# Kernel optimization log

Measured on AMD Instinct MI355X. Metric: run time of the kernel, lower is better.

## Reference

```python
import jax, jax.numpy as jnp
import numpy as np

H = 2048
V = 32000
B = 4            # 2 chosen + 2 rejected sequences
T = 1024
BETA = 0.1
IGNORE_INDEX = -100


def setup_inputs() -> dict:
    key = jax.random.key(0)
    k1, k2, k3, k4, k5 = jax.random.split(key, 5)
    x = jax.random.normal(k1, (B, T, H), dtype=jnp.float32)
    ref_x = jax.random.normal(k2, (B, T, H), dtype=jnp.float32)
    y = jax.random.randint(k3, (B, T), 0, V, dtype=jnp.int64)
    # Linear weights scaled ~1/sqrt(H) so logits are well-conditioned
    W = jax.random.normal(k4, (V, H), dtype=jnp.float32) * (1.0 / np.sqrt(H))
    W_ref = jax.random.normal(k5, (V, H), dtype=jnp.float32) * (1.0 / np.sqrt(H))
    return {"x": x, "ref_x": ref_x, "y": y, "W": W, "W_ref": W_ref}


def _avg_seq_logps(h, W, y, mask):
    # h: [B,T,H], W: [V,H] -> average per-sequence log-prob of the target tokens
    logits = jnp.einsum("bth,vh->btv", h, W)                 # [B,T,V]
    logps = jax.nn.log_softmax(logits, axis=-1)
    y_safe = jnp.where(mask, y, 0)
    per_tok = jnp.take_along_axis(logps, y_safe[..., None], axis=-1)[..., 0]  # [B,T]
    m = mask.astype(logps.dtype)
    return (per_tok * m).sum(-1) / m.sum(-1)                  # [B]


def reference(x, ref_x, y, W, W_ref):
    mask = y != IGNORE_INDEX
    logps = _avg_seq_logps(x, W, y, mask)
    # reference model path is computed without gradients (torch.no_grad in Liger)
    ref_logps = jax.lax.stop_gradient(_avg_seq_logps(ref_x, W_ref, y, mask))
    half = B // 2
    chosen, rejected = logps[:half], logps[half:]
    ref_chosen, ref_rejected = ref_logps[:half], ref_logps[half:]
    logits_diff = BETA * ((chosen - ref_chosen) - (rejected - ref_rejected))
    loss = -jax.nn.log_sigmoid(logits_diff).sum() / half
    return loss
```

## Files before the change

### kernel.cpp

```cpp
#include <hip/hip_runtime.h>
#include <cstdint>
#include <cstddef>

#define HDIM 2048
#define VOCAB 32000
#define BT 4096
#define NVB 125
#define BETA_F 0.1f
#define SCALE_X 16.0f
#define SCALE_W 64.0f
#define INV_SC (1.0f / (SCALE_X * SCALE_W))

typedef float f32x4 __attribute__((ext_vector_type(4)));
typedef long lx2 __attribute__((ext_vector_type(2)));

__device__ __forceinline__ void async_lds16(const void* g, void* l) {
  __builtin_amdgcn_global_load_lds(
      (__attribute__((address_space(1))) void*)g,
      (__attribute__((address_space(3))) void*)l,
      16, 0, 0);
}

#define BAR() __builtin_amdgcn_s_barrier()
#define SCHED0() __builtin_amdgcn_sched_barrier(0)
#define VMCNT(n) do { asm volatile("s_waitcnt vmcnt(" #n ")" ::: "memory"); \
                      __builtin_amdgcn_sched_barrier(0); } while (0)

__global__ void cast_fp8_kernel(const float* __restrict__ src,
                                uint4* __restrict__ dst, int n16, float scale) {
  int i = blockIdx.x * blockDim.x + threadIdx.x;
  int stride = gridDim.x * blockDim.x;
  for (; i < n16; i += stride) {
    const float4* s = (const float4*)src + (size_t)i * 4;
    uint4 o;
    {
      float4 a = s[0];
      int r = __builtin_amdgcn_cvt_pk_fp8_f32(a.x * scale, a.y * scale, 0, false);
      o.x = __builtin_amdgcn_cvt_pk_fp8_f32(a.z * scale, a.w * scale, r, true);
    }
    {
      float4 a = s[1];
      int r = __builtin_amdgcn_cvt_pk_fp8_f32(a.x * scale, a.y * scale, 0, false);
      o.y = __builtin_amdgcn_cvt_pk_fp8_f32(a.z * scale, a.w * scale, r, true);
    }
    {
      float4 a = s[2];
      int r = __builtin_amdgcn_cvt_pk_fp8_f32(a.x * scale, a.y * scale, 0, false);
      o.z = __builtin_amdgcn_cvt_pk_fp8_f32(a.z * scale, a.w * scale, r, true);
    }
    {
      float4 a = s[3];
      int r = __builtin_amdgcn_cvt_pk_fp8_f32(a.x * scale, a.y * scale, 0, false);
      o.w = __builtin_amdgcn_cvt_pk_fp8_f32(a.z * scale, a.w * scale, r, true);
    }
    dst[i] = o;
  }
}

__global__ __launch_bounds__(1024) void gemm_lse256(
    const unsigned char* __restrict__ Xq,
    const unsigned char* __restrict__ Xrq,
    const unsigned char* __restrict__ Wq,
    const unsigned char* __restrict__ Wrq,
    float2* __restrict__ part) {
  __shared__ __align__(16) char lds[4][2][2][8192];

  const int tid = threadIdx.x;
  const int lane = tid & 63;
  const int w = tid >> 6;
  const int wm = w >> 2;
  const int wn = w & 3;
  const int which = blockIdx.y;

  const int lin = blockIdx.x;
  const int nl = (lin & 7) * 250 + (lin >> 3);
  const int mb = nl & 15;
  const int nb = nl >> 4;

  const unsigned char* A = which ? Xrq : Xq;
  const unsigned char* B = which ? Wrq : Wq;
  float2* pp = part + (size_t)which * BT * NVB;

  const int lanep = lane ^ ((lane & 32) >> 4);
  const int srow = (w >> 3) * 128 + (w & 7) * 16 + (lanep >> 2);
  const int scol = (lanep & 3) * 16;
  const unsigned char* Ag = A + (size_t)(mb * 256 + srow) * HDIM + scol;
  const unsigned char* Bg = B + (size_t)(nb * 256 + srow) * HDIM + scol;

#define STAGE_AB(buf, T) do {                                                 \
    int _t = (T) > 31 ? 31 : (T);                                             \
    async_lds16(Ag + (size_t)_t * 64, &lds[buf][0][0][0] + w * 1024);         \
    async_lds16(Bg + (size_t)_t * 64, &lds[buf][1][0][0] + w * 1024);         \
  } while (0)

  const int l15 = lane & 15;
  const int kbyte = (lane >> 4) * 16;
#define FRAGP(d0, d1, halfptr, row) do {                                      \
    int _r = (row);                                                           \
    int _L = _r * 64 + kbyte;                                                 \
    lx2 _v = *(const lx2*)((halfptr) + (_L ^ (((_r >> 3) & 1) << 5)));        \
    d0 = _v.x; d1 = _v.y;                                                     \
  } while (0)

  const char* Ah[4] = { &lds[0][0][wm >> 1][0], &lds[1][0][wm >> 1][0],
                        &lds[2][0][wm >> 1][0], &lds[3][0][wm >> 1][0] };
  const char* Bh[4] = { &lds[0][1][wn >> 1][0], &lds[1][1][wn >> 1][0],
                        &lds[2][1][wn >> 1][0], &lds[3][1][wn >> 1][0] };
  const int arow = (wm & 1) * 64 + l15;
  const int brow = (wn & 1) * 64 + l15;

  f32x4 acc[4][4] = {};
  long aLo[2][2], aHi[2][2], bLo[2][2], bHi[2][2];

#define RD_ALO(buf) do {                                                      \
    _Pragma("unroll") for (int mi = 0; mi < 2; ++mi)                          \
      FRAGP(aLo[mi][0], aLo[mi][1], Ah[buf], arow + mi * 16);                 \
  } while (0)
#define RD_AHI(buf) do {                                                      \
    _Pragma("unroll") for (int mi = 0; mi < 2; ++mi)                          \
      FRAGP(aHi[mi][0], aHi[mi][1], Ah[buf], arow + (2 + mi) * 16);           \
  } while (0)
#define RD_B01(buf) do {                                                      \
    _Pragma("unroll") for (int ni = 0; ni < 2; ++ni)                          \
      FRAGP(bLo[ni][0], bLo[ni][1], Bh[buf], brow + ni * 16);                 \
  } while (0)
#define RD_B23(buf) do {                                                      \
    _Pragma("unroll") for (int ni = 0; ni < 2; ++ni)                          \
      FRAGP(bHi[ni][0], bHi[ni][1], Bh[buf], brow + (2 + ni) * 16);           \
  } while (0)
#define MFMA_Q(AG, BG, MI0, NI0) do {                                         \
    __builtin_amdgcn_s_setprio(1);                                            \
    _Pragma("unroll") for (int kk = 0; kk < 2; ++kk)                          \
    _Pragma("unroll") for (int mi = 0; mi < 2; ++mi)                          \
    _Pragma("unroll") for (int ni = 0; ni < 2; ++ni)                          \
      acc[(MI0) + mi][(NI0) + ni] = __builtin_amdgcn_mfma_f32_16x16x32_fp8_fp8( \
          AG[mi][kk], BG[ni][kk], acc[(MI0) + mi][(NI0) + ni], 0, 0, 0);      \
    __builtin_amdgcn_s_setprio(0);                                            \
  } while (0)

#define TILE(C, CN, ST) do {                                                  \
    RD_B23(C); SCHED0();                                                      \
    MFMA_Q(aLo, bLo, 0, 0); SCHED0();                                         \
    STAGE_AB((C + 3) & 3, ST);                                                \
    RD_AHI(C); SCHED0();                                                      \
    MFMA_Q(aLo, bHi, 0, 2); SCHED0();                                         \
    MFMA_Q(aHi, bLo, 2, 0); SCHED0();                                         \
    VMCNT(4);                     \
    BAR(); SCHED0();                                                          \
    RD_ALO(CN); RD_B01(CN); SCHED0();                                         \
    MFMA_Q(aHi, bHi, 2, 2); SCHED0();                                         \
  } while (0)

  STAGE_AB(0, 0);
  STAGE_AB(1, 1);
  STAGE_AB(2, 2);
  VMCNT(4);
  BAR(); SCHED0();
  RD_ALO(0); RD_B01(0);
  SCHED0();

  for (int i = 0; i < 8; ++i) {
    const int base = 4 * i;
    TILE(0, 1, base + 3);
    TILE(1, 2, base + 4);
    TILE(2, 3, base + 5);
    TILE(3, 0, base + 6);
  }
  VMCNT(0);
  BAR(); SCHED0();

  float* red = (float*)&lds[0][0][0][0];
#pragma unroll
  for (int mi = 0; mi < 4; ++mi) {
#pragma unroll
    for (int r = 0; r < 4; ++r) {
      float v0 = acc[mi][0][r] * INV_SC;
      float v1 = acc[mi][1][r] * INV_SC;
      float v2 = acc[mi][2][r] * INV_SC;
      float v3 = acc[mi][3][r] * INV_SC;
      float m = fmaxf(fmaxf(v0, v1), fmaxf(v2, v3));
#pragma unroll
      for (int o = 1; o < 16; o <<= 1) m = fmaxf(m, __shfl_xor(m, o, 64));
      float s = __expf(v0 - m) + __expf(v1 - m) + __expf(v2 - m) + __expf(v3 - m);
#pragma unroll
      for (int o = 1; o < 16; o <<= 1) s += __shfl_xor(s, o, 64);
      if (l15 == 0) {
        int row = wm * 64 + mi * 16 + (lane >> 4) * 4 + r;
        red[wn * 256 + row] = m;
        red[1024 + wn * 256 + row] = s;
      }
    }
  }
  __syncthreads();
  if (tid < 256) {
    float m0 = red[tid], m1 = red[256 + tid], m2 = red[512 + tid], m3 = red[768 + tid];
    float M = fmaxf(fmaxf(m0, m1), fmaxf(m2, m3));
    float S = red[1024 + tid] * __expf(m0 - M) + red[1280 + tid] * __expf(m1 - M) +
              red[1536 + tid] * __expf(m2 - M) + red[1792 + tid] * __expf(m3 - M);
    pp[(size_t)(mb * 256 + tid) * NVB + nb] = make_float2(M, S);
  }
#undef STAGE_AB
#undef FRAGP
#undef RD_ALO
#undef RD_AHI
#undef RD_B01
#undef RD_B23
#undef MFMA_Q
#undef TILE
}

__global__ void target_logit(const float* __restrict__ x, const float* __restrict__ xr,
                             const float* __restrict__ W, const float* __restrict__ Wr,
                             const int* __restrict__ y, float* __restrict__ tlog) {
  int wid = (blockIdx.x * blockDim.x + threadIdx.x) >> 6;
  int lane = threadIdx.x & 63;
  int which = wid >> 12;
  int tok = wid & 4095;
  int yy = y[tok];
  int ys = (yy == -100) ? 0 : yy;
  const float* xv = (which ? xr : x) + (size_t)tok * HDIM;
  const float* wv = (which ? Wr : W) + (size_t)ys * HDIM;
  const float4* x4 = (const float4*)xv;
  const float4* w4 = (const float4*)wv;
  float sum = 0.f;
  for (int i = lane; i < HDIM / 4; i += 64) {
    float4 a = x4[i], b = w4[i];
    sum += a.x * b.x + a.y * b.y + a.z * b.z + a.w * b.w;
  }
#pragma unroll
  for (int o = 1; o < 64; o <<= 1) sum += __shfl_xor(sum, o, 64);
  if (lane == 0) tlog[wid] = sum;
}

__global__ void lse_combine(const float2* __restrict__ part,
                            const float* __restrict__ tlog,
                            float* __restrict__ ptok) {
  int wid = (blockIdx.x * blockDim.x + threadIdx.x) >> 6;
  int lane = threadIdx.x & 63;
  const float2* p = part + (size_t)wid * NVB;
  float m = -INFINITY, s = 0.f;
  for (int i = lane; i < NVB; i += 64) {
    float2 v = p[i];
    float M = fmaxf(m, v.x);
    s = s * __expf(m - M) + v.y * __expf(v.x - M);
    m = M;
  }
#pragma unroll
  for (int o = 1; o < 64; o <<= 1) {
    float mo = __shfl_xor(m, o, 64);
    float so = __shfl_xor(s, o, 64);
    float M = fmaxf(m, mo);
    s = s * __expf(m - M) + so * __expf(mo - M);
    m = M;
  }
  if (lane == 0) ptok[wid] = tlog[wid] - (m + logf(s));
}

__global__ void final_loss(const float* __restrict__ ptok,
                           const int* __restrict__ y, float* __restrict__ out) {
  __shared__ float rs[256];
  __shared__ float rc[256];
  __shared__ float seq[8];
  int tid = threadIdx.x;
  for (int s = 0; s < 8; ++s) {
    int which = s >> 2, b = s & 3;
    float lsum = 0.f, lcnt = 0.f;
    for (int t = tid; t < 1024; t += 256) {
      int yy = y[b * 1024 + t];
      if (yy != -100) {
        lsum += ptok[which * 4096 + b * 1024 + t];
        lcnt += 1.f;
      }
    }
    rs[tid] = lsum; rc[tid] = lcnt;
    __syncthreads();
    for (int o = 128; o > 0; o >>= 1) {
      if (tid < o) { rs[tid] += rs[tid + o]; rc[tid] += rc[tid + o]; }
      __syncthreads();
    }
    if (tid == 0) seq[s] = rs[0] / rc[0];
    __syncthreads();
  }
  if (tid == 0) {
    float d0 = BETA_F * ((seq[0] - seq[4]) - (seq[2] - seq[6]));
    float d1 = BETA_F * ((seq[1] - seq[5]) - (seq[3] - seq[7]));
    auto sp = [](float a) { return fmaxf(a, 0.f) + log1pf(expf(-fabsf(a))); };
    out[0] = (sp(-d0) + sp(-d1)) * 0.5f;
  }
}

extern "C" void kernel_launch(void* const* d_in, const int* in_sizes, int n_in,
                              void* d_out, int out_size, void* d_ws, size_t ws_size,
                              hipStream_t stream) {
  const float* x   = (const float*)d_in[0];
  const float* xr  = (const float*)d_in[1];
  const int*   y   = (const int*)d_in[2];
  const float* Wf  = (const float*)d_in[3];
  const float* Wrf = (const float*)d_in[4];
  float* out = (float*)d_out;

  char* ws = (char*)d_ws;
  size_t off = 0;
  auto alloc = [&](size_t bytes) -> void* {
    void* p = ws + off;
    off = (off + bytes + 255) & ~(size_t)255;
    return p;
  };
  unsigned char* Xq  = (unsigned char*)alloc((size_t)BT * HDIM);
  unsigned char* Xrq = (unsigned char*)alloc((size_t)BT * HDIM);
  unsigned char* Wq  = (unsigned char*)alloc((size_t)VOCAB * HDIM);
  unsigned char* Wrq = (unsigned char*)alloc((size_t)VOCAB * HDIM);
  float2* part = (float2*)alloc((size_t)2 * BT * NVB * sizeof(float2));
  float*  tlog = (float*)alloc((size_t)2 * BT * sizeof(float));
  float*  ptok = (float*)alloc((size_t)2 * BT * sizeof(float));

  cast_fp8_kernel<<<2048, 256, 0, stream>>>(x,  (uint4*)Xq,  BT * HDIM / 16, SCALE_X);
  cast_fp8_kernel<<<2048, 256, 0, stream>>>(xr, (uint4*)Xrq, BT * HDIM / 16, SCALE_X);
  cast_fp8_kernel<<<2048, 256, 0, stream>>>(Wf,  (uint4*)Wq,  VOCAB * HDIM / 16, SCALE_W);
  cast_fp8_kernel<<<2048, 256, 0, stream>>>(Wrf, (uint4*)Wrq, VOCAB * HDIM / 16, SCALE_W);

  dim3 gg(2000, 2);
  gemm_lse256<<<gg, 1024, 0, stream>>>(Xq, Xrq, Wq, Wrq, part);

  target_logit<<<2048, 256, 0, stream>>>(x, xr, Wf, Wrf, y, tlog);
  lse_combine<<<2048, 256, 0, stream>>>(part, tlog, ptok);
  final_loss<<<1, 256, 0, stream>>>(ptok, y, out);
}
```

Baseline: 1.111 ms.

## Switch GEMM pipeline from 4-stage K=64 ring to 2-stage K=128 double buffer

Replaces the four-deep LDS ring of 64-byte K slices with a two-deep double buffer of 128-byte K super-tiles. Each super-tile issues four async loads and runs twice the MFMA work between barriers, so there are half as many barriers and vmcnt waits. In exchange the prefetch distance shrinks to one super-tile and the wait is now a full vmcnt(0), which may expose more global-load latency.

```diff
diff --git a/kernel.cpp b/kernel.cpp
--- a/kernel.cpp
+++ b/kernel.cpp
@@ -63,7 +63,7 @@
     const unsigned char* __restrict__ Wq,
     const unsigned char* __restrict__ Wrq,
     float2* __restrict__ part) {
-  __shared__ __align__(16) char lds[4][2][2][8192];
+  __shared__ __align__(16) char lds[2][2][2][16384];
 
   const int tid = threadIdx.x;
   const int lane = tid & 63;
@@ -87,10 +87,11 @@
   const unsigned char* Ag = A + (size_t)(mb * 256 + srow) * HDIM + scol;
   const unsigned char* Bg = B + (size_t)(nb * 256 + srow) * HDIM + scol;
 
-#define STAGE_AB(buf, T) do {                                                 \
-    int _t = (T) > 31 ? 31 : (T);                                             \
-    async_lds16(Ag + (size_t)_t * 64, &lds[buf][0][0][0] + w * 1024);         \
-    async_lds16(Bg + (size_t)_t * 64, &lds[buf][1][0][0] + w * 1024);         \
+#define STAGE4(buf, T) do {                                                   \
+    async_lds16(Ag + (size_t)(2 * (T)) * 64,     &lds[buf][0][0][0] + w * 1024); \
+    async_lds16(Ag + (size_t)(2 * (T) + 1) * 64, &lds[buf][0][1][0] + w * 1024); \
+    async_lds16(Bg + (size_t)(2 * (T)) * 64,     &lds[buf][1][0][0] + w * 1024); \
+    async_lds16(Bg + (size_t)(2 * (T) + 1) * 64, &lds[buf][1][1][0] + w * 1024); \
   } while (0)
 
   const int l15 = lane & 15;
@@ -102,31 +103,31 @@
     d0 = _v.x; d1 = _v.y;                                                     \
   } while (0)
 
-  const char* Ah[4] = { &lds[0][0][wm >> 1][0], &lds[1][0][wm >> 1][0],
-                        &lds[2][0][wm >> 1][0], &lds[3][0][wm >> 1][0] };
-  const char* Bh[4] = { &lds[0][1][wn >> 1][0], &lds[1][1][wn >> 1][0],
-                        &lds[2][1][wn >> 1][0], &lds[3][1][wn >> 1][0] };
+  const int ahalf = (wm >> 1) * 8192;
+  const int bhalf = (wn >> 1) * 8192;
+#define APTR(buf, sub) (&lds[buf][0][sub][0] + ahalf)
+#define BPTR(buf, sub) (&lds[buf][1][sub][0] + bhalf)
   const int arow = (wm & 1) * 64 + l15;
   const int brow = (wn & 1) * 64 + l15;
 
   f32x4 acc[4][4] = {};
   long aLo[2][2], aHi[2][2], bLo[2][2], bHi[2][2];
 
-#define RD_ALO(buf) do {                                                      \
+#define RD_ALO(buf, sub) do {                                                 \
     _Pragma("unroll") for (int mi = 0; mi < 2; ++mi)                          \
-      FRAGP(aLo[mi][0], aLo[mi][1], Ah[buf], arow + mi * 16);                 \
-  } while (0)
-#define RD_AHI(buf) do {                                                      \
+      FRAGP(aLo[mi][0], aLo[mi][1], APTR(buf, sub), arow + mi * 16);          \
+  } while (0)
+#define RD_AHI(buf, sub) do {                                                 \
     _Pragma("unroll") for (int mi = 0; mi < 2; ++mi)                          \
-      FRAGP(aHi[mi][0], aHi[mi][1], Ah[buf], arow + (2 + mi) * 16);           \
-  } while (0)
-#define RD_B01(buf) do {                                                      \
+      FRAGP(aHi[mi][0], aHi[mi][1], APTR(buf, sub), arow + (2 + mi) * 16);    \
+  } while (0)
+#define RD_B01(buf, sub) do {                                                 \
     _Pragma("unroll") for (int ni = 0; ni < 2; ++ni)                          \
-      FRAGP(bLo[ni][0], bLo[ni][1], Bh[buf], brow + ni * 16);                 \
-  } while (0)
-#define RD_B23(buf) do {                                                      \
+      FRAGP(bLo[ni][0], bLo[ni][1], BPTR(buf, sub), brow + ni * 16);          \
+  } while (0)
+#define RD_B23(buf, sub) do {                                                 \
     _Pragma("unroll") for (int ni = 0; ni < 2; ++ni)                          \
-      FRAGP(bHi[ni][0], bHi[ni][1], Bh[buf], brow + (2 + ni) * 16);           \
+      FRAGP(bHi[ni][0], bHi[ni][1], BPTR(buf, sub), brow + (2 + ni) * 16);    \
   } while (0)
 #define MFMA_Q(AG, BG, MI0, NI0) do {                                         \
     __builtin_amdgcn_s_setprio(1);                                            \
@@ -138,33 +139,37 @@
     __builtin_amdgcn_s_setprio(0);                                            \
   } while (0)
 
-#define TILE(C, CN, ST) do {                                                  \
-    RD_B23(C); SCHED0();                                                      \
+#define SUPER(C, NB, T) do {                                                  \
+    STAGE4(NB, T); SCHED0();                                                  \
+    RD_B23(C, 0); SCHED0();                                                   \
     MFMA_Q(aLo, bLo, 0, 0); SCHED0();                                         \
-    STAGE_AB((C + 3) & 3, ST);                                                \
-    RD_AHI(C); SCHED0();                                                      \
+    RD_AHI(C, 0); SCHED0();                                                   \
     MFMA_Q(aLo, bHi, 0, 2); SCHED0();                                         \
     MFMA_Q(aHi, bLo, 2, 0); SCHED0();                                         \
-    VMCNT(4);                     \
+    RD_ALO(C, 1); RD_B01(C, 1); SCHED0();                                     \
+    MFMA_Q(aHi, bHi, 2, 2); SCHED0();                                         \
+    RD_B23(C, 1); SCHED0();                                                   \
+    MFMA_Q(aLo, bLo, 0, 0); SCHED0();                                         \
+    RD_AHI(C, 1); SCHED0();                                                   \
+    MFMA_Q(aLo, bHi, 0, 2); SCHED0();                                         \
+    MFMA_Q(aHi, bLo, 2, 0); SCHED0();                                         \
+    VMCNT(0);                                                                 \
     BAR(); SCHED0();                                                          \
-    RD_ALO(CN); RD_B01(CN); SCHED0();                                         \
+    RD_ALO(NB, 0); RD_B01(NB, 0); SCHED0();                                   \
     MFMA_Q(aHi, bHi, 2, 2); SCHED0();                                         \
   } while (0)
 
-  STAGE_AB(0, 0);
-  STAGE_AB(1, 1);
-  STAGE_AB(2, 2);
-  VMCNT(4);
+  STAGE4(0, 0);
+  VMCNT(0);
   BAR(); SCHED0();
-  RD_ALO(0); RD_B01(0);
+  RD_ALO(0, 0); RD_B01(0, 0);
   SCHED0();
 
-  for (int i = 0; i < 8; ++i) {
-    const int base = 4 * i;
-    TILE(0, 1, base + 3);
-    TILE(1, 2, base + 4);
-    TILE(2, 3, base + 5);
-    TILE(3, 0, base + 6);
+  for (int j = 0; j < 8; ++j) {
+    const int t1 = 2 * j + 1;
+    const int t2 = (2 * j + 2 > 15) ? 15 : 2 * j + 2;
+    SUPER(0, 1, t1);
+    SUPER(1, 0, t2);
   }
   VMCNT(0);
   BAR(); SCHED0();
@@ -199,14 +204,16 @@
               red[1536 + tid] * __expf(m2 - M) + red[1792 + tid] * __expf(m3 - M);
     pp[(size_t)(mb * 256 + tid) * NVB + nb] = make_float2(M, S);
   }
-#undef STAGE_AB
+#undef STAGE4
 #undef FRAGP
+#undef APTR
+#undef BPTR
 #undef RD_ALO
 #undef RD_AHI
 #undef RD_B01
 #undef RD_B23
 #undef MFMA_Q
-#undef TILE
+#undef SUPER
 }
 
 __global__ void target_logit(const float* __restrict__ x, const float* __restrict__ xr,
```

After: 951.2 us. 14.4% less time.
